# Performance work log

Hardware: AMD Instinct MI355X
Metric: run time of the kernel (lower is better)

Reference implementation:

```python
import jax, jax.numpy as jnp
import numpy as np
from jax import lax

WINDOW_SIZE = 11
SIGMA = 1.5
DATA_RANGE = 1.0


def gaussian_window(size, sigma):
    k = jnp.arange(size, dtype=jnp.float32) - size // 2
    k = jnp.exp(-0.5 / sigma ** 2 * k ** 2)
    return k / k.sum()


def depthwise_conv(x, window):
    # x: [B,C,H,W], window: [C,1,k,k]
    pad = WINDOW_SIZE // 2
    return lax.conv_general_dilated(
        x, window,
        window_strides=(1, 1),
        padding=[(pad, pad), (pad, pad)],
        dimension_numbers=('NCHW', 'OIHW', 'NCHW'),
        feature_group_count=x.shape[1])


def setup_inputs() -> dict:
    key = jax.random.key(0)
    k1, k2 = jax.random.split(key)
    img1 = jax.random.uniform(k1, (32, 3, 512, 512), dtype=jnp.float32)
    img2 = jax.random.uniform(k2, (32, 3, 512, 512), dtype=jnp.float32)
    return {"img1": img1, "img2": img2}


def reference(img1, img2):
    channels = img1.shape[1]
    w1 = gaussian_window(WINDOW_SIZE, SIGMA)[:, None]        # [k,1]
    w2 = w1 @ w1.T                                           # [k,k]
    window = jnp.broadcast_to(w2, (channels, 1, WINDOW_SIZE, WINDOW_SIZE))

    C1 = (0.01 * DATA_RANGE) ** 2
    C2 = (0.03 * DATA_RANGE) ** 2

    mu1 = depthwise_conv(img1, window)
    mu2 = depthwise_conv(img2, window)
    mu1_sq = mu1 * mu1
    mu2_sq = mu2 * mu2
    mu1_mu2 = mu1 * mu2
    sigma1_sq = depthwise_conv(img1 * img1, window) - mu1_sq
    sigma2_sq = depthwise_conv(img2 * img2, window) - mu2_sq
    sigma12 = depthwise_conv(img1 * img2, window) - mu1_mu2

    ssim_map = ((2 * mu1_mu2 + C1) * (2 * sigma12 + C2)) / (
        (mu1_sq + mu2_sq + C1) * (sigma1_sq + sigma2_sq + C2))
    return 1.0 - ssim_map.mean()
```

## Files before the change

kernel.cpp:

```cpp
#include <hip/hip_runtime.h>
#include <math.h>

typedef _Float16 f16;
typedef f16 f16x8 __attribute__((ext_vector_type(8)));
typedef f16 f16x2 __attribute__((ext_vector_type(2)));
typedef float f32x4 __attribute__((ext_vector_type(4)));
typedef unsigned int u32;
typedef u32 u32x2 __attribute__((ext_vector_type(2)));

constexpr int H = 512, W = 512;
constexpr int TY = 16;
constexpr int NBANDS = H / TY;
constexpr int NPLANES = 96;
constexpr int NB = NBANDS * NPLANES;
constexpr int VP = 552;
constexpr double NTOT = 25165824.0;
constexpr float C1 = 1.0e-4f;
constexpr float C2 = 9.0e-4f;

struct Wts { float w[11]; };

__device__ __forceinline__ u32 pk(float lo, float hi) {
    return __builtin_bit_cast(u32, __builtin_amdgcn_cvt_pkrtz(lo, hi));
}

__global__ __launch_bounds__(512, 4)
void ssim_main(const float* __restrict__ img1, const float* __restrict__ img2,
               float* __restrict__ part, Wts wts)
{
    __shared__ __align__(16) f16 vc[4][TY][VP];
    __shared__ __align__(16) f16 Tb[16][40];
    __shared__ float red[8];

    const int tid  = threadIdx.x;
    const int lane = tid & 63;
    const int wave = tid >> 6;
    const int tr   = lane & 15;
    const int g    = lane >> 4;
    const int k0   = g * 8;

    for (int i = tid; i < 640; i += 512) {
        const int m = i / 40, k = i - m * 40, d = k - m;
        Tb[m][k] = (d >= 0 && d <= 10) ? (f16)wts.w[d] : (f16)0.0f;
    }
    __syncthreads();
    const f16x8 tw = *(const f16x8*)&Tb[tr][k0];

    const int band = blockIdx.x;
    const int y0   = band * TY;
    const size_t plane = (size_t)blockIdx.y * (size_t)(H * W);
    const float* p1 = img1 + plane;
    const float* p2 = img2 + plane;

    int   rowbase[8];
    float ymul[8];
    #pragma unroll
    for (int j = 0; j < 8; ++j) {
        const int y = y0 - 5 + k0 + j;
        const bool yok = (unsigned)y < (unsigned)H;
        rowbase[j] = (yok ? y : 0) * W;
        ymul[j] = yok ? 1.f : 0.f;
    }

    const f32x4 z4 = { 0.f, 0.f, 0.f, 0.f };

    for (int t = wave; t < 33; t += 8) {
        const int x   = 16 * t + tr - 5;
        const bool xok = (unsigned)x < (unsigned)W;
        const int xc  = xok ? x : 0;
        const float xm = xok ? 1.f : 0.f;

        f16x8 fA, fB, fQa, fQb;
        #pragma unroll
        for (int j = 0; j < 8; ++j) {
            const float m  = xm * ymul[j];
            const float a1 = p1[rowbase[j] + xc] * m;
            const float a2 = p2[rowbase[j] + xc] * m;
            const float a = a1 + a2, b = a1 - a2;
            fA[j]  = (f16)a;        fB[j]  = (f16)b;
            fQa[j] = (f16)(a * a);  fQb[j] = (f16)(b * b);
        }
        const f32x4 dA  = __builtin_amdgcn_mfma_f32_16x16x32_f16(fA,  tw, z4, 0, 0, 0);
        const f32x4 dB  = __builtin_amdgcn_mfma_f32_16x16x32_f16(fB,  tw, z4, 0, 0, 0);
        const f32x4 dQa = __builtin_amdgcn_mfma_f32_16x16x32_f16(fQa, tw, z4, 0, 0, 0);
        const f32x4 dQb = __builtin_amdgcn_mfma_f32_16x16x32_f16(fQb, tw, z4, 0, 0, 0);

        const int cb = 16 * t + 4 * g;
        { u32x2 v = { pk(dA[0],  dA[1]),  pk(dA[2],  dA[3])  }; *(u32x2*)&vc[0][tr][cb] = v; }
        { u32x2 v = { pk(dB[0],  dB[1]),  pk(dB[2],  dB[3])  }; *(u32x2*)&vc[1][tr][cb] = v; }
        { u32x2 v = { pk(dQa[0], dQa[1]), pk(dQa[2], dQa[3]) }; *(u32x2*)&vc[2][tr][cb] = v; }
        { u32x2 v = { pk(dQb[0], dQb[1]), pk(dQb[2], dQb[3]) }; *(u32x2*)&vc[3][tr][cb] = v; }
    }
    __syncthreads();

    float local = 0.f;
    for (int t = wave; t < 32; t += 8) {
        const int cb = 16 * t;
        const f16x8 bA  = *(const f16x8*)&vc[0][tr][cb + k0];
        const f16x8 bB  = *(const f16x8*)&vc[1][tr][cb + k0];
        const f16x8 bQa = *(const f16x8*)&vc[2][tr][cb + k0];
        const f16x8 bQb = *(const f16x8*)&vc[3][tr][cb + k0];
        const f32x4 rA  = __builtin_amdgcn_mfma_f32_16x16x32_f16(tw, bA,  z4, 0, 0, 0);
        const f32x4 rB  = __builtin_amdgcn_mfma_f32_16x16x32_f16(tw, bB,  z4, 0, 0, 0);
        const f32x4 rQa = __builtin_amdgcn_mfma_f32_16x16x32_f16(tw, bQa, z4, 0, 0, 0);
        const f32x4 rQb = __builtin_amdgcn_mfma_f32_16x16x32_f16(tw, bQb, z4, 0, 0, 0);

        #pragma unroll
        for (int i = 0; i < 4; ++i) {
            const float A  = rA[i],  Bv = rB[i];
            const float Qa = rQa[i], Qb = rQb[i];
            const float u = A * A, v = Bv * Bv;
            const float t1 = u - v;
            const float t2 = u + v;
            const float num1 = fmaf(0.5f, t1, C1);
            const float den1 = fmaf(0.5f, t2, C1);
            const float num2 = fmaf(0.5f, (Qa - Qb) - t1, C2);
            const float den2 = fmaf(0.5f, (Qa + Qb) - t2, C2);
            local += (num1 * num2) * __builtin_amdgcn_rcpf(den1 * den2);
        }
    }

    #pragma unroll
    for (int off = 32; off > 0; off >>= 1) local += __shfl_down(local, off, 64);
    if (lane == 0) red[wave] = local;
    __syncthreads();
    if (tid == 0) {
        float s = 0.f;
        #pragma unroll
        for (int wv = 0; wv < 8; ++wv) s += red[wv];
        part[blockIdx.y * NBANDS + band] = s;
    }
}

__global__ __launch_bounds__(512)
void ssim_final(const float* __restrict__ part, float* __restrict__ out)
{
    __shared__ double red[8];
    const int tid = threadIdx.x;
    double s = 0.0;
    for (int i = tid; i < NB; i += 512) s += (double)part[i];
    #pragma unroll
    for (int off = 32; off > 0; off >>= 1) s += __shfl_down(s, off, 64);
    if ((tid & 63) == 0) red[tid >> 6] = s;
    __syncthreads();
    if (tid == 0) {
        double t = 0.0;
        #pragma unroll
        for (int wv = 0; wv < 8; ++wv) t += red[wv];
        out[0] = (float)(1.0 - t / NTOT);
    }
}

extern "C" void kernel_launch(void* const* d_in, const int* in_sizes, int n_in,
                              void* d_out, int out_size, void* d_ws, size_t ws_size,
                              hipStream_t stream)
{
    const float* img1 = (const float*)d_in[0];
    const float* img2 = (const float*)d_in[1];
    float* out = (float*)d_out;
    float* part = (float*)d_ws;

    Wts wts;
    double wd[11], s = 0.0;
    for (int k = 0; k < 11; ++k) {
        const double d = (double)(k - 5);
        wd[k] = exp(-0.5 / (1.5 * 1.5) * d * d);
        s += wd[k];
    }
    for (int k = 0; k < 11; ++k) wts.w[k] = (float)(wd[k] / s);

    dim3 grid(NBANDS, NPLANES);
    ssim_main<<<grid, 512, 0, stream>>>(img1, img2, part, wts);
    ssim_final<<<1, 512, 0, stream>>>(part, out);
}
```

Before: 227.1 us.

## Split bands into half-width tiles, specialize edge masking, swizzle block order

Each block now covers a 16x256 tile instead of a full 512-wide band, which halves LDS use and raises the launch-bounds occupancy hint from 4 to 8 blocks. The grid becomes 1D with an XCD-style swizzle of block indices. Template specializations drop the x/y boundary masking for interior tiles. Loads for the always-zero padding rows (k>=26) are skipped and values are packed with cvt_pkrtz. The cost is extra halo recomputation, since each tile now processes 17 column tiles for 16 outputs, and more partial sums to reduce.

```diff
diff --git a/kernel.cpp b/kernel.cpp
--- a/kernel.cpp
+++ b/kernel.cpp
@@ -3,17 +3,21 @@
 
 typedef _Float16 f16;
 typedef f16 f16x8 __attribute__((ext_vector_type(8)));
-typedef f16 f16x2 __attribute__((ext_vector_type(2)));
 typedef float f32x4 __attribute__((ext_vector_type(4)));
 typedef unsigned int u32;
 typedef u32 u32x2 __attribute__((ext_vector_type(2)));
+typedef u32 u32x4 __attribute__((ext_vector_type(4)));
 
 constexpr int H = 512, W = 512;
 constexpr int TY = 16;
+constexpr int TW = 256;
 constexpr int NBANDS = H / TY;
+constexpr int GXB = W / TW;
 constexpr int NPLANES = 96;
-constexpr int NB = NBANDS * NPLANES;
-constexpr int VP = 552;
+constexpr int NBLK = GXB * NBANDS * NPLANES;
+constexpr int NTILES_V = 17;
+constexpr int NTILES_H = TW / 16;
+constexpr int VP = 280;
 constexpr double NTOT = 25165824.0;
 constexpr float C1 = 1.0e-4f;
 constexpr float C2 = 9.0e-4f;
@@ -24,7 +28,87 @@
     return __builtin_bit_cast(u32, __builtin_amdgcn_cvt_pkrtz(lo, hi));
 }
 
-__global__ __launch_bounds__(512, 4)
+template<bool MASK, bool YEDGE>
+__device__ __forceinline__ void stage_v(const float* __restrict__ p1,
+                                        const float* __restrict__ p2,
+                                        f16 (&vc)[4][TY][VP], const f16x8 tw,
+                                        const int (&rowbase)[8], const float (&ymul)[8],
+                                        int x, int t, int tr, int g, int k0)
+{
+    int xc = x; float xm = 1.f;
+    if (MASK) {
+        const bool xok = (unsigned)x < (unsigned)W;
+        xc = xok ? x : 0;
+        xm = xok ? 1.f : 0.f;
+    }
+    u32 pa[4], pb[4], pqa[4], pqb[4];
+    #pragma unroll
+    for (int jp = 0; jp < 4; ++jp) {
+        float a0 = 0.f, b0 = 0.f, q0 = 0.f, r0 = 0.f;
+        float a1 = 0.f, b1 = 0.f, q1 = 0.f, r1 = 0.f;
+        if (k0 + 2 * jp < 26) {
+            const int j0 = 2 * jp, j1 = 2 * jp + 1;
+            float v1a = p1[rowbase[j0] + xc], v2a = p2[rowbase[j0] + xc];
+            float v1b = p1[rowbase[j1] + xc], v2b = p2[rowbase[j1] + xc];
+            if (MASK || YEDGE) {
+                float m0 = 1.f, m1 = 1.f;
+                if (MASK)  { m0 = xm; m1 = xm; }
+                if (YEDGE) { m0 *= ymul[j0]; m1 *= ymul[j1]; }
+                v1a *= m0; v2a *= m0; v1b *= m1; v2b *= m1;
+            }
+            a0 = v1a + v2a; b0 = v1a - v2a; q0 = a0 * a0; r0 = b0 * b0;
+            a1 = v1b + v2b; b1 = v1b - v2b; q1 = a1 * a1; r1 = b1 * b1;
+        }
+        pa[jp]  = pk(a0, a1);  pb[jp]  = pk(b0, b1);
+        pqa[jp] = pk(q0, q1);  pqb[jp] = pk(r0, r1);
+    }
+    const f16x8 fA  = __builtin_bit_cast(f16x8, (u32x4){pa[0],  pa[1],  pa[2],  pa[3]});
+    const f16x8 fB  = __builtin_bit_cast(f16x8, (u32x4){pb[0],  pb[1],  pb[2],  pb[3]});
+    const f16x8 fQa = __builtin_bit_cast(f16x8, (u32x4){pqa[0], pqa[1], pqa[2], pqa[3]});
+    const f16x8 fQb = __builtin_bit_cast(f16x8, (u32x4){pqb[0], pqb[1], pqb[2], pqb[3]});
+
+    const f32x4 z4 = { 0.f, 0.f, 0.f, 0.f };
+    const f32x4 dA  = __builtin_amdgcn_mfma_f32_16x16x32_f16(fA,  tw, z4, 0, 0, 0);
+    const f32x4 dB  = __builtin_amdgcn_mfma_f32_16x16x32_f16(fB,  tw, z4, 0, 0, 0);
+    const f32x4 dQa = __builtin_amdgcn_mfma_f32_16x16x32_f16(fQa, tw, z4, 0, 0, 0);
+    const f32x4 dQb = __builtin_amdgcn_mfma_f32_16x16x32_f16(fQb, tw, z4, 0, 0, 0);
+
+    const int cb = 16 * t + 4 * g;
+    { u32x2 v = { pk(dA[0],  dA[1]),  pk(dA[2],  dA[3])  }; *(u32x2*)&vc[0][tr][cb] = v; }
+    { u32x2 v = { pk(dB[0],  dB[1]),  pk(dB[2],  dB[3])  }; *(u32x2*)&vc[1][tr][cb] = v; }
+    { u32x2 v = { pk(dQa[0], dQa[1]), pk(dQa[2], dQa[3]) }; *(u32x2*)&vc[2][tr][cb] = v; }
+    { u32x2 v = { pk(dQb[0], dQb[1]), pk(dQb[2], dQb[3]) }; *(u32x2*)&vc[3][tr][cb] = v; }
+}
+
+template<bool YEDGE>
+__device__ __forceinline__ void stage_v_all(const float* __restrict__ p1,
+                                            const float* __restrict__ p2,
+                                            f16 (&vc)[4][TY][VP], const f16x8 tw,
+                                            int y0, int x0, int xb,
+                                            int tr, int g, int k0, int wave)
+{
+    int rowbase[8]; float ymul[8];
+    #pragma unroll
+    for (int j = 0; j < 8; ++j) {
+        const int y = y0 - 5 + k0 + j;
+        if (YEDGE) {
+            const bool yok = (unsigned)y < (unsigned)H;
+            rowbase[j] = (yok ? y : 0) * W;
+            ymul[j] = yok ? 1.f : 0.f;
+        } else {
+            rowbase[j] = y * W;
+            ymul[j] = 1.f;
+        }
+    }
+    const int mt = xb ? (NTILES_V - 1) : 0;
+    for (int t = wave; t < NTILES_V; t += 8) {
+        const int x = x0 + 16 * t + tr - 5;
+        if (t == mt) stage_v<true,  YEDGE>(p1, p2, vc, tw, rowbase, ymul, x, t, tr, g, k0);
+        else         stage_v<false, YEDGE>(p1, p2, vc, tw, rowbase, ymul, x, t, tr, g, k0);
+    }
+}
+
+__global__ __launch_bounds__(512, 8)
 void ssim_main(const float* __restrict__ img1, const float* __restrict__ img2,
                float* __restrict__ part, Wts wts)
 {
@@ -46,56 +130,30 @@
     __syncthreads();
     const f16x8 tw = *(const f16x8*)&Tb[tr][k0];
 
-    const int band = blockIdx.x;
-    const int y0   = band * TY;
-    const size_t plane = (size_t)blockIdx.y * (size_t)(H * W);
-    const float* p1 = img1 + plane;
-    const float* p2 = img2 + plane;
-
-    int   rowbase[8];
-    float ymul[8];
-    #pragma unroll
-    for (int j = 0; j < 8; ++j) {
-        const int y = y0 - 5 + k0 + j;
-        const bool yok = (unsigned)y < (unsigned)H;
-        rowbase[j] = (yok ? y : 0) * W;
-        ymul[j] = yok ? 1.f : 0.f;
-    }
+    const int id    = blockIdx.x;
+    const int gb    = (id & 7) * (NBLK / 8) + (id >> 3);
+    const int plane = gb >> 6;
+    const int rem   = gb & 63;
+    const int band  = rem >> 1;
+    const int xb    = rem & 1;
+
+    const int y0 = band * TY;
+    const int x0 = xb * TW;
+    const size_t poff = (size_t)plane * (size_t)(H * W);
+    const float* p1 = img1 + poff;
+    const float* p2 = img2 + poff;
+
+    if (band == 0 || band == NBANDS - 1)
+        stage_v_all<true>(p1, p2, vc, tw, y0, x0, xb, tr, g, k0, wave);
+    else
+        stage_v_all<false>(p1, p2, vc, tw, y0, x0, xb, tr, g, k0, wave);
+    __syncthreads();
 
     const f32x4 z4 = { 0.f, 0.f, 0.f, 0.f };
-
-    for (int t = wave; t < 33; t += 8) {
-        const int x   = 16 * t + tr - 5;
-        const bool xok = (unsigned)x < (unsigned)W;
-        const int xc  = xok ? x : 0;
-        const float xm = xok ? 1.f : 0.f;
-
-        f16x8 fA, fB, fQa, fQb;
-        #pragma unroll
-        for (int j = 0; j < 8; ++j) {
-            const float m  = xm * ymul[j];
-            const float a1 = p1[rowbase[j] + xc] * m;
-            const float a2 = p2[rowbase[j] + xc] * m;
-            const float a = a1 + a2, b = a1 - a2;
-            fA[j]  = (f16)a;        fB[j]  = (f16)b;
-            fQa[j] = (f16)(a * a);  fQb[j] = (f16)(b * b);
-        }
-        const f32x4 dA  = __builtin_amdgcn_mfma_f32_16x16x32_f16(fA,  tw, z4, 0, 0, 0);
-        const f32x4 dB  = __builtin_amdgcn_mfma_f32_16x16x32_f16(fB,  tw, z4, 0, 0, 0);
-        const f32x4 dQa = __builtin_amdgcn_mfma_f32_16x16x32_f16(fQa, tw, z4, 0, 0, 0);
-        const f32x4 dQb = __builtin_amdgcn_mfma_f32_16x16x32_f16(fQb, tw, z4, 0, 0, 0);
-
-        const int cb = 16 * t + 4 * g;
-        { u32x2 v = { pk(dA[0],  dA[1]),  pk(dA[2],  dA[3])  }; *(u32x2*)&vc[0][tr][cb] = v; }
-        { u32x2 v = { pk(dB[0],  dB[1]),  pk(dB[2],  dB[3])  }; *(u32x2*)&vc[1][tr][cb] = v; }
-        { u32x2 v = { pk(dQa[0], dQa[1]), pk(dQa[2], dQa[3]) }; *(u32x2*)&vc[2][tr][cb] = v; }
-        { u32x2 v = { pk(dQb[0], dQb[1]), pk(dQb[2], dQb[3]) }; *(u32x2*)&vc[3][tr][cb] = v; }
-    }
-    __syncthreads();
-
     float local = 0.f;
-    for (int t = wave; t < 32; t += 8) {
-        const int cb = 16 * t;
+    #pragma unroll
+    for (int i = 0; i < NTILES_H / 8; ++i) {
+        const int cb = 16 * (wave + 8 * i);
         const f16x8 bA  = *(const f16x8*)&vc[0][tr][cb + k0];
         const f16x8 bB  = *(const f16x8*)&vc[1][tr][cb + k0];
         const f16x8 bQa = *(const f16x8*)&vc[2][tr][cb + k0];
@@ -106,9 +164,9 @@
         const f32x4 rQb = __builtin_amdgcn_mfma_f32_16x16x32_f16(tw, bQb, z4, 0, 0, 0);
 
         #pragma unroll
-        for (int i = 0; i < 4; ++i) {
-            const float A  = rA[i],  Bv = rB[i];
-            const float Qa = rQa[i], Qb = rQb[i];
+        for (int e = 0; e < 4; ++e) {
+            const float A  = rA[e],  Bv = rB[e];
+            const float Qa = rQa[e], Qb = rQb[e];
             const float u = A * A, v = Bv * Bv;
             const float t1 = u - v;
             const float t2 = u + v;
@@ -128,7 +186,7 @@
         float s = 0.f;
         #pragma unroll
         for (int wv = 0; wv < 8; ++wv) s += red[wv];
-        part[blockIdx.y * NBANDS + band] = s;
+        part[id] = s;
     }
 }
 
@@ -138,7 +196,7 @@
     __shared__ double red[8];
     const int tid = threadIdx.x;
     double s = 0.0;
-    for (int i = tid; i < NB; i += 512) s += (double)part[i];
+    for (int i = tid; i < NBLK; i += 512) s += (double)part[i];
     #pragma unroll
     for (int off = 32; off > 0; off >>= 1) s += __shfl_down(s, off, 64);
     if ((tid & 63) == 0) red[tid >> 6] = s;
@@ -169,7 +227,6 @@
     }
     for (int k = 0; k < 11; ++k) wts.w[k] = (float)(wd[k] / s);
 
-    dim3 grid(NBANDS, NPLANES);
-    ssim_main<<<grid, 512, 0, stream>>>(img1, img2, part, wts);
+    ssim_main<<<NBLK, 512, 0, stream>>>(img1, img2, part, wts);
     ssim_final<<<1, 512, 0, stream>>>(part, out);
 }
```

Result: slower. 468.3 us (+106.2%).
